# Kernel optimization log

Measured on AMD Instinct MI355X. Metric: run time of the kernel, lower is better.

Reference implementation:

```python
import jax, jax.numpy as jnp
import numpy as np

B, S, E, H = 4, 2048, 1024, 16
HD = E // H  # head_dim = 64
EPS = 1.1920928955078125e-07  # torch.finfo(float32).eps (RMSNorm eps=None default)


def _rmsnorm(x, w):
    # normalize over last dim
    ms = jnp.mean(x * x, axis=-1, keepdims=True)
    return x * jax.lax.rsqrt(ms + EPS) * w


def _rope(x, start_pos=0):
    # x: [B, H, S, HD]; interleaved (even/odd) rotary embedding
    seq_len = x.shape[-2]
    inv_freq = 1.0 / (10000.0 ** (jnp.arange(0, HD, 2, dtype=jnp.float32) / HD))  # [HD/2]
    t = jnp.arange(start_pos, start_pos + seq_len, dtype=jnp.float32)  # [S]
    freqs = t[:, None] * inv_freq[None, :]  # [S, HD/2]
    cos = jnp.cos(freqs)[None, None]  # [1,1,S,HD/2]
    sin = jnp.sin(freqs)[None, None]
    x1 = x[..., 0::2]
    x2 = x[..., 1::2]
    o1 = x1 * cos - x2 * sin
    o2 = x1 * sin + x2 * cos
    # stack(..., -1).flatten(-2) -> re-interleave
    return jnp.stack((o1, o2), axis=-1).reshape(x.shape)


def setup_inputs() -> dict:
    key = jax.random.key(0)
    k1, k2, k3, k4 = jax.random.split(key, 4)
    lim = 1.0 / np.sqrt(E)
    return {
        "q": jax.random.normal(k1, (B, S, E), jnp.float32),
        "k": jax.random.normal(k2, (B, S, E), jnp.float32),
        "v": jax.random.normal(k3, (B, S, E), jnp.float32),
        "q_norm_w": jnp.ones((HD,), jnp.float32),
        "k_norm_w": jnp.ones((HD,), jnp.float32),
        "proj_w": jax.random.uniform(k4, (E, E), jnp.float32, -lim, lim),
        "proj_b": jnp.zeros((E,), jnp.float32),
    }


def reference(q, k, v, q_norm_w, k_norm_w, proj_w, proj_b):
    b, s, _ = q.shape
    scale = HD ** -0.5
    # [B,S,E] -> [B,H,S,HD]
    qh = q.reshape(b, s, H, HD).transpose(0, 2, 1, 3)
    kh = k.reshape(b, s, H, HD).transpose(0, 2, 1, 3)
    vh = v.reshape(b, s, H, HD).transpose(0, 2, 1, 3)
    # per-head QK RMSNorm then RoPE
    qh = _rope(_rmsnorm(qh, q_norm_w))
    kh = _rope(_rmsnorm(kh, k_norm_w))
    # explicit attention (no mask path)
    scores = jnp.einsum("bhqd,bhkd->bhqk", qh, kh) * scale  # [B,H,S,S]
    attn = jax.nn.softmax(scores, axis=-1)
    ctx = jnp.einsum("bhqk,bhkd->bhqd", attn, vh)
    ctx = ctx.transpose(0, 2, 1, 3).reshape(b, s, E)
    return ctx @ proj_w.T + proj_b
```

## Files before the change

kernel.cpp:

```cpp
#include <hip/hip_runtime.h>
#include <hip/hip_bf16.h>
#include <cstdint>

#define B_ 4
#define S_ 2048
#define E_ 1024
#define H_ 16
#define HD_ 64
#define EPS_ 1.1920928955078125e-07f

typedef __attribute__((ext_vector_type(8))) short shortx8;
typedef __attribute__((ext_vector_type(4))) float floatx4;
typedef __attribute__((ext_vector_type(8))) _Float16 halfx8;
typedef __attribute__((ext_vector_type(2))) __fp16 fp16x2;

#define C1_ 0.18033688068389154f

__global__ __launch_bounds__(256) void prep(
    const float* __restrict__ q, const float* __restrict__ k,
    const float* __restrict__ v,
    const float* __restrict__ qw, const float* __restrict__ kw,
    const float* __restrict__ pw,
    __hip_bfloat16* __restrict__ qh, __hip_bfloat16* __restrict__ kh,
    _Float16* __restrict__ vt, __hip_bfloat16* __restrict__ wb)
{
    __shared__ _Float16 tile[64][72];
    const int bid = blockIdx.x;
    const int tid = threadIdx.x;

    if (bid < 16384) {
        const size_t PT = (size_t)B_ * S_ * E_ / 4;
        size_t t = (size_t)bid * 256 + tid;
        const bool is_k = (t >= PT);
        if (is_k) t -= PT;

        const int row = (int)(t >> 8);
        const int b   = row / S_;
        const int s   = row % S_;
        const int grp = (int)(t & 255);
        const int h   = grp >> 4;
        const int dl  = (grp & 15) * 4;

        const float* __restrict__ src = is_k ? k : q;
        const float* __restrict__ w   = is_k ? kw : qw;
        __hip_bfloat16* __restrict__ dst = is_k ? kh : qh;

        const float4 x  = ((const float4*)src)[t];
        const float4 wv = ((const float4*)w)[grp & 15];

        float ss = x.x * x.x + x.y * x.y + x.z * x.z + x.w * x.w;
#pragma unroll
        for (int m = 1; m < 16; m <<= 1) ss += __shfl_xor(ss, m);
        float r = rsqrtf(ss * (1.0f / HD_) + EPS_);
        if (!is_k) r *= C1_;

        const float xn0 = x.x * r * wv.x;
        const float xn1 = x.y * r * wv.y;
        const float xn2 = x.z * r * wv.z;
        const float xn3 = x.w * r * wv.w;

        const float L2I = 0.41524101186092029f;
        const int   i0  = dl >> 1;
        const float f0  = (float)s * __builtin_amdgcn_exp2f(-(float)i0 * L2I);
        const float f1  = (float)s * __builtin_amdgcn_exp2f(-(float)(i0 + 1) * L2I);
        const float c0 = __cosf(f0), sn0 = __sinf(f0);
        const float c1 = __cosf(f1), sn1 = __sinf(f1);

        __hip_bfloat16 pk[4];
        pk[0] = __float2bfloat16(xn0 * c0 - xn1 * sn0);
        pk[1] = __float2bfloat16(xn0 * sn0 + xn1 * c0);
        pk[2] = __float2bfloat16(xn2 * c1 - xn3 * sn1);
        pk[3] = __float2bfloat16(xn2 * sn1 + xn3 * c1);
        *(ushort4*)(dst + ((size_t)((b * H_ + h) * S_ + s)) * HD_ + dl) =
            *(const ushort4*)pk;
    } else if (bid < 18432) {
        const int bb2 = bid - 16384;
        const int s0  = (bb2 & 31) * 64;
        const int bh  = bb2 >> 5;
        const int b   = bh >> 4, h = bh & 15;
        {
            const int sl = tid >> 2;
            const int o  = sl;
            const int n  = (o & 32) | (((o >> 2) & 3) << 3) |
                           (((o >> 4) & 1) << 2) | (o & 3);
            const int d0 = (tid & 3) * 16;
            const float* __restrict__ src =
                v + ((size_t)(b * S_ + s0 + sl)) * E_ + h * HD_ + d0;
            float4 f0 = ((const float4*)src)[0];
            float4 f1 = ((const float4*)src)[1];
            float4 f2 = ((const float4*)src)[2];
            float4 f3 = ((const float4*)src)[3];
            float vals[16] = {f0.x,f0.y,f0.z,f0.w, f1.x,f1.y,f1.z,f1.w,
                              f2.x,f2.y,f2.z,f2.w, f3.x,f3.y,f3.z,f3.w};
#pragma unroll
            for (int j = 0; j < 16; ++j)
                tile[d0 + j][n] = (_Float16)vals[j];
        }
        __syncthreads();
        {
            const int d  = tid >> 2;
            const int sg = (tid & 3) * 16;
            _Float16* __restrict__ dst =
                vt + ((size_t)(bh * HD_ + d)) * S_ + s0 + sg;
            ((uint4*)dst)[0] = *(const uint4*)&tile[d][sg];
            ((uint4*)dst)[1] = *(const uint4*)&tile[d][sg + 8];
        }
    } else {
        const int i = (bid - 18432) * 256 + tid;
        float4 f = ((const float4*)pw)[i];
        wb[4 * i + 0] = __float2bfloat16(f.x);
        wb[4 * i + 1] = __float2bfloat16(f.y);
        wb[4 * i + 2] = __float2bfloat16(f.z);
        wb[4 * i + 3] = __float2bfloat16(f.w);
    }
}

__global__ __launch_bounds__(256, 4) void attn(
    const __hip_bfloat16* __restrict__ qh, const __hip_bfloat16* __restrict__ kh,
    const _Float16* __restrict__ vt, __hip_bfloat16* __restrict__ ctx)
{
    __shared__ __hip_bfloat16 Kt[128][72];
    __shared__ _Float16       Vt[64][152];

    const int bid  = blockIdx.x;
    const int slot = bid >> 3;
    const int bh   = ((bid & 7) << 3) | (slot & 7);
    const int q0   = (slot >> 3) * 128;
    const int tid  = threadIdx.x;
    const int wv   = tid >> 6;
    const int lane = tid & 63;
    const int l16  = lane & 15;
    const int quad = lane >> 4;
    const int b    = bh >> 4, h = bh & 15;

    shortx8 aq[2][2];
#pragma unroll
    for (int mh = 0; mh < 2; ++mh) {
        const __hip_bfloat16* qbase =
            qh + ((size_t)bh * S_ + q0 + wv * 32 + mh * 16 + l16) * HD_;
        aq[mh][0] = *(const shortx8*)(qbase + quad * 8);
        aq[mh][1] = *(const shortx8*)(qbase + 32 + quad * 8);
    }

    const halfx8 ones = {(_Float16)1.f, (_Float16)1.f, (_Float16)1.f, (_Float16)1.f,
                         (_Float16)1.f, (_Float16)1.f, (_Float16)1.f, (_Float16)1.f};

    floatx4 O[2][4] = {};
    floatx4 O5[2]   = {};

    const __hip_bfloat16* __restrict__ kbase = kh + (size_t)bh * S_ * HD_;
    const _Float16* __restrict__ vbase = vt + (size_t)bh * HD_ * S_;

    const int sr = tid >> 1, sc = (tid & 1) * 32;
    const int vr = tid >> 2, vc = (tid & 3) * 32;

    uint4 gk0, gk1, gk2, gk3, gv0, gv1, gv2, gv3;
    {
        const uint4* kp = (const uint4*)(kbase + (size_t)sr * HD_ + sc);
        gk0 = kp[0]; gk1 = kp[1]; gk2 = kp[2]; gk3 = kp[3];
        const uint4* vp = (const uint4*)(vbase + (size_t)vr * S_ + vc);
        gv0 = vp[0]; gv1 = vp[1]; gv2 = vp[2]; gv3 = vp[3];
    }

    for (int kt = 0; kt < S_ / 128; ++kt) {
        *(uint4*)&Kt[sr][sc]      = gk0;
        *(uint4*)&Kt[sr][sc + 8]  = gk1;
        *(uint4*)&Kt[sr][sc + 16] = gk2;
        *(uint4*)&Kt[sr][sc + 24] = gk3;
        *(uint4*)&Vt[vr][vc]      = gv0;
        *(uint4*)&Vt[vr][vc + 8]  = gv1;
        *(uint4*)&Vt[vr][vc + 16] = gv2;
        *(uint4*)&Vt[vr][vc + 24] = gv3;
        __syncthreads();

        if (kt + 1 < S_ / 128) {
            const uint4* kp = (const uint4*)(kbase +
                (size_t)((kt + 1) * 128 + sr) * HD_ + sc);
            gk0 = kp[0]; gk1 = kp[1]; gk2 = kp[2]; gk3 = kp[3];
        }

#pragma unroll
        for (int hk = 0; hk < 2; ++hk) {
            floatx4 s4[2][4];
            __builtin_amdgcn_s_setprio(1);
#pragma unroll
            for (int nt = 0; nt < 4; ++nt) {
                const shortx8 kb0 =
                    *(const shortx8*)&Kt[hk * 64 + nt * 16 + l16][quad * 8];
                const shortx8 kb1 =
                    *(const shortx8*)&Kt[hk * 64 + nt * 16 + l16][32 + quad * 8];
#pragma unroll
                for (int mh = 0; mh < 2; ++mh) {
                    floatx4 c = {0.f, 0.f, 0.f, 0.f};
                    c = __builtin_amdgcn_mfma_f32_16x16x32_bf16(kb0, aq[mh][0], c, 0, 0, 0);
                    c = __builtin_amdgcn_mfma_f32_16x16x32_bf16(kb1, aq[mh][1], c, 0, 0, 0);
                    s4[mh][nt] = c;
                }
            }
            __builtin_amdgcn_s_setprio(0);

            halfx8 bb[2][2];
#pragma unroll
            for (int mh = 0; mh < 2; ++mh)
#pragma unroll
                for (int f = 0; f < 2; ++f) {
                    union { fp16x2 h2[4]; halfx8 h8; } u;
                    u.h2[0] = __builtin_amdgcn_cvt_pkrtz(
                        __builtin_amdgcn_exp2f(s4[mh][2 * f][0]),
                        __builtin_amdgcn_exp2f(s4[mh][2 * f][1]));
                    u.h2[1] = __builtin_amdgcn_cvt_pkrtz(
                        __builtin_amdgcn_exp2f(s4[mh][2 * f][2]),
                        __builtin_amdgcn_exp2f(s4[mh][2 * f][3]));
                    u.h2[2] = __builtin_amdgcn_cvt_pkrtz(
                        __builtin_amdgcn_exp2f(s4[mh][2 * f + 1][0]),
                        __builtin_amdgcn_exp2f(s4[mh][2 * f + 1][1]));
                    u.h2[3] = __builtin_amdgcn_cvt_pkrtz(
                        __builtin_amdgcn_exp2f(s4[mh][2 * f + 1][2]),
                        __builtin_amdgcn_exp2f(s4[mh][2 * f + 1][3]));
                    bb[mh][f] = u.h8;
                }

            if (hk == 0 && kt + 1 < S_ / 128) {
                const uint4* vp = (const uint4*)(vbase +
                    (size_t)vr * S_ + (kt + 1) * 128 + vc);
                gv0 = vp[0]; gv1 = vp[1]; gv2 = vp[2]; gv3 = vp[3];
            }

            __builtin_amdgcn_s_setprio(1);
#pragma unroll
            for (int mh = 0; mh < 2; ++mh) {
                O5[mh] = __builtin_amdgcn_mfma_f32_16x16x32_f16(ones, bb[mh][0], O5[mh], 0, 0, 0);
                O5[mh] = __builtin_amdgcn_mfma_f32_16x16x32_f16(ones, bb[mh][1], O5[mh], 0, 0, 0);
            }

#pragma unroll
            for (int dt = 0; dt < 4; ++dt) {
                const _Float16* vrow = &Vt[dt * 16 + l16][hk * 64];
                const halfx8 A0 = *(const halfx8*)(vrow + quad * 8);
                const halfx8 A1 = *(const halfx8*)(vrow + 32 + quad * 8);
#pragma unroll
                for (int mh = 0; mh < 2; ++mh) {
                    O[mh][dt] = __builtin_amdgcn_mfma_f32_16x16x32_f16(
                        A0, bb[mh][0], O[mh][dt], 0, 0, 0);
                    O[mh][dt] = __builtin_amdgcn_mfma_f32_16x16x32_f16(
                        A1, bb[mh][1], O[mh][dt], 0, 0, 0);
                }
            }
            __builtin_amdgcn_s_setprio(0);
        }
        __syncthreads();
    }

#pragma unroll
    for (int mh = 0; mh < 2; ++mh) {
        const float inv = 1.0f / O5[mh][0];
        const int s = q0 + wv * 32 + mh * 16 + l16;
        __hip_bfloat16* cb = ctx + ((size_t)(b * S_ + s)) * E_ + h * HD_;
#pragma unroll
        for (int dt = 0; dt < 4; ++dt) {
            __hip_bfloat16 pk[4];
#pragma unroll
            for (int r = 0; r < 4; ++r)
                pk[r] = __float2bfloat16(O[mh][dt][r] * inv);
            *(ushort4*)(cb + dt * 16 + quad * 4) = *(const ushort4*)pk;
        }
    }
}

__global__ __launch_bounds__(256) void proj(
    const __hip_bfloat16* __restrict__ ctx, const __hip_bfloat16* __restrict__ wb,
    const float* __restrict__ bias, float* __restrict__ out)
{
    __shared__ __hip_bfloat16 As[128][72];
    __shared__ __hip_bfloat16 Bs[128][72];

    const int bid  = blockIdx.x;
    const int slot = bid >> 3;
    const int mblk = ((bid & 7) << 3) | (slot & 7);
    const int nblk = slot >> 3;
    const int m0 = mblk * 128;
    const int n0 = nblk * 128;
    const int tid  = threadIdx.x;
    const int wv   = tid >> 6;
    const int lane = tid & 63;
    const int l16  = lane & 15;
    const int quad = lane >> 4;
    const int wr   = (wv >> 1) * 64;
    const int wc   = (wv & 1) * 64;

    const int srow = tid >> 1;
    const int scol = (tid & 1) * 32;

    floatx4 acc[4][4] = {};

    for (int k0 = 0; k0 < E_; k0 += 64) {
        const uint4* ap = (const uint4*)(ctx + (size_t)(m0 + srow) * E_ + k0 + scol);
        const uint4* bp = (const uint4*)(wb  + (size_t)(n0 + srow) * E_ + k0 + scol);
        uint4 a0 = ap[0], a1 = ap[1], a2 = ap[2], a3 = ap[3];
        uint4 b0 = bp[0], b1 = bp[1], b2 = bp[2], b3 = bp[3];
        *(uint4*)&As[srow][scol]      = a0;
        *(uint4*)&As[srow][scol + 8]  = a1;
        *(uint4*)&As[srow][scol + 16] = a2;
        *(uint4*)&As[srow][scol + 24] = a3;
        *(uint4*)&Bs[srow][scol]      = b0;
        *(uint4*)&Bs[srow][scol + 8]  = b1;
        *(uint4*)&Bs[srow][scol + 16] = b2;
        *(uint4*)&Bs[srow][scol + 24] = b3;
        __syncthreads();

#pragma unroll
        for (int ks = 0; ks < 2; ++ks) {
            shortx8 af[4], bf[4];
#pragma unroll
            for (int mt = 0; mt < 4; ++mt)
                af[mt] = *(const shortx8*)&As[wr + mt * 16 + l16][ks * 32 + quad * 8];
#pragma unroll
            for (int nt = 0; nt < 4; ++nt)
                bf[nt] = *(const shortx8*)&Bs[wc + nt * 16 + l16][ks * 32 + quad * 8];

#pragma unroll
            for (int mt = 0; mt < 4; ++mt)
#pragma unroll
                for (int nt = 0; nt < 4; ++nt)
                    acc[mt][nt] = __builtin_amdgcn_mfma_f32_16x16x32_bf16(
                        af[mt], bf[nt], acc[mt][nt], 0, 0, 0);
        }
        __syncthreads();
    }

#pragma unroll
    for (int nt = 0; nt < 4; ++nt) {
        const float bv = bias[n0 + wc + nt * 16 + l16];
#pragma unroll
        for (int mt = 0; mt < 4; ++mt)
#pragma unroll
            for (int r = 0; r < 4; ++r) {
                const int mrow = m0 + wr + mt * 16 + quad * 4 + r;
                const int ncol = n0 + wc + nt * 16 + l16;
                out[(size_t)mrow * E_ + ncol] = acc[mt][nt][r] + bv;
            }
    }
}

extern "C" void kernel_launch(void* const* d_in, const int* in_sizes, int n_in,
                              void* d_out, int out_size, void* d_ws, size_t ws_size,
                              hipStream_t stream)
{
    const float* q  = (const float*)d_in[0];
    const float* k  = (const float*)d_in[1];
    const float* v  = (const float*)d_in[2];
    const float* qw = (const float*)d_in[3];
    const float* kw = (const float*)d_in[4];
    const float* pw = (const float*)d_in[5];
    const float* pb = (const float*)d_in[6];
    float* out = (float*)d_out;

    char* ws = (char*)d_ws;
    const size_t SEG = (size_t)B_ * H_ * S_ * HD_ * 2;
    __hip_bfloat16* qh  = (__hip_bfloat16*)(ws);
    __hip_bfloat16* kh  = (__hip_bfloat16*)(ws + SEG);
    _Float16*       vt  = (_Float16*)(ws + 2 * SEG);
    __hip_bfloat16* ctx = (__hip_bfloat16*)(ws + 3 * SEG);
    __hip_bfloat16* wbp = (__hip_bfloat16*)(ws + 4 * SEG);

    prep<<<dim3(19456), 256, 0, stream>>>(q, k, v, qw, kw, pw, qh, kh, vt, wbp);
    attn<<<dim3(1024), 256, 0, stream>>>(qh, kh, vt, ctx);
    proj<<<dim3(512), 256, 0, stream>>>(ctx, wbp, pb, out);
}
```

Measured before the change: 273.1 us.

## Drop register prefetch of K/V tiles and interleave QK MFMA with exp per half

Removes the register-staged prefetch of the next K and V tiles. Each iteration now loads its K/V tile from global memory and stores it straight to LDS before the barrier. The QK score computation is also split into two halves, so the exp/convert of one half follows its MFMAs directly. The aim is to lower register pressure and gain occupancy or interleave MFMA with transcendental work. The cost is exposed global load latency, since loads no longer overlap compute within a wave.

Result: faster. 248.1 us (-9.2%).

```diff
diff --git a/kernel.cpp b/kernel.cpp
--- a/kernel.cpp
+++ b/kernel.cpp
@@ -154,76 +154,67 @@
     const int sr = tid >> 1, sc = (tid & 1) * 32;
     const int vr = tid >> 2, vc = (tid & 3) * 32;
 
-    uint4 gk0, gk1, gk2, gk3, gv0, gv1, gv2, gv3;
-    {
-        const uint4* kp = (const uint4*)(kbase + (size_t)sr * HD_ + sc);
-        gk0 = kp[0]; gk1 = kp[1]; gk2 = kp[2]; gk3 = kp[3];
-        const uint4* vp = (const uint4*)(vbase + (size_t)vr * S_ + vc);
-        gv0 = vp[0]; gv1 = vp[1]; gv2 = vp[2]; gv3 = vp[3];
-    }
-
     for (int kt = 0; kt < S_ / 128; ++kt) {
-        *(uint4*)&Kt[sr][sc]      = gk0;
-        *(uint4*)&Kt[sr][sc + 8]  = gk1;
-        *(uint4*)&Kt[sr][sc + 16] = gk2;
-        *(uint4*)&Kt[sr][sc + 24] = gk3;
-        *(uint4*)&Vt[vr][vc]      = gv0;
-        *(uint4*)&Vt[vr][vc + 8]  = gv1;
-        *(uint4*)&Vt[vr][vc + 16] = gv2;
-        *(uint4*)&Vt[vr][vc + 24] = gv3;
-        __syncthreads();
-
-        if (kt + 1 < S_ / 128) {
+        {
             const uint4* kp = (const uint4*)(kbase +
-                (size_t)((kt + 1) * 128 + sr) * HD_ + sc);
-            gk0 = kp[0]; gk1 = kp[1]; gk2 = kp[2]; gk3 = kp[3];
-        }
+                (size_t)(kt * 128 + sr) * HD_ + sc);
+            uint4 k0 = kp[0], k1 = kp[1], k2 = kp[2], k3 = kp[3];
+            *(uint4*)&Kt[sr][sc]      = k0;
+            *(uint4*)&Kt[sr][sc + 8]  = k1;
+            *(uint4*)&Kt[sr][sc + 16] = k2;
+            *(uint4*)&Kt[sr][sc + 24] = k3;
+        }
+        {
+            const uint4* vp = (const uint4*)(vbase +
+                (size_t)vr * S_ + kt * 128 + vc);
+            uint4 v0 = vp[0], v1 = vp[1], v2 = vp[2], v3 = vp[3];
+            *(uint4*)&Vt[vr][vc]      = v0;
+            *(uint4*)&Vt[vr][vc + 8]  = v1;
+            *(uint4*)&Vt[vr][vc + 16] = v2;
+            *(uint4*)&Vt[vr][vc + 24] = v3;
+        }
+        __syncthreads();
 
 #pragma unroll
         for (int hk = 0; hk < 2; ++hk) {
-            floatx4 s4[2][4];
-            __builtin_amdgcn_s_setprio(1);
-#pragma unroll
-            for (int nt = 0; nt < 4; ++nt) {
-                const shortx8 kb0 =
-                    *(const shortx8*)&Kt[hk * 64 + nt * 16 + l16][quad * 8];
-                const shortx8 kb1 =
-                    *(const shortx8*)&Kt[hk * 64 + nt * 16 + l16][32 + quad * 8];
+            halfx8 bb[2][2];
+#pragma unroll
+            for (int f = 0; f < 2; ++f) {
+                floatx4 s4p[2][2];
+                __builtin_amdgcn_s_setprio(1);
+#pragma unroll
+                for (int nt2 = 0; nt2 < 2; ++nt2) {
+                    const int nt = 2 * f + nt2;
+                    const shortx8 kb0 =
+                        *(const shortx8*)&Kt[hk * 64 + nt * 16 + l16][quad * 8];
+                    const shortx8 kb1 =
+                        *(const shortx8*)&Kt[hk * 64 + nt * 16 + l16][32 + quad * 8];
+#pragma unroll
+                    for (int mh = 0; mh < 2; ++mh) {
+                        floatx4 c = {0.f, 0.f, 0.f, 0.f};
+                        c = __builtin_amdgcn_mfma_f32_16x16x32_bf16(kb0, aq[mh][0], c, 0, 0, 0);
+                        c = __builtin_amdgcn_mfma_f32_16x16x32_bf16(kb1, aq[mh][1], c, 0, 0, 0);
+                        s4p[mh][nt2] = c;
+                    }
+                }
+                __builtin_amdgcn_s_setprio(0);
 #pragma unroll
                 for (int mh = 0; mh < 2; ++mh) {
-                    floatx4 c = {0.f, 0.f, 0.f, 0.f};
-                    c = __builtin_amdgcn_mfma_f32_16x16x32_bf16(kb0, aq[mh][0], c, 0, 0, 0);
-                    c = __builtin_amdgcn_mfma_f32_16x16x32_bf16(kb1, aq[mh][1], c, 0, 0, 0);
-                    s4[mh][nt] = c;
-                }
-            }
-            __builtin_amdgcn_s_setprio(0);
-
-            halfx8 bb[2][2];
-#pragma unroll
-            for (int mh = 0; mh < 2; ++mh)
-#pragma unroll
-                for (int f = 0; f < 2; ++f) {
                     union { fp16x2 h2[4]; halfx8 h8; } u;
                     u.h2[0] = __builtin_amdgcn_cvt_pkrtz(
-                        __builtin_amdgcn_exp2f(s4[mh][2 * f][0]),
-                        __builtin_amdgcn_exp2f(s4[mh][2 * f][1]));
+                        __builtin_amdgcn_exp2f(s4p[mh][0][0]),
+                        __builtin_amdgcn_exp2f(s4p[mh][0][1]));
                     u.h2[1] = __builtin_amdgcn_cvt_pkrtz(
-                        __builtin_amdgcn_exp2f(s4[mh][2 * f][2]),
-                        __builtin_amdgcn_exp2f(s4[mh][2 * f][3]));
+                        __builtin_amdgcn_exp2f(s4p[mh][0][2]),
+                        __builtin_amdgcn_exp2f(s4p[mh][0][3]));
                     u.h2[2] = __builtin_amdgcn_cvt_pkrtz(
-                        __builtin_amdgcn_exp2f(s4[mh][2 * f + 1][0]),
-                        __builtin_amdgcn_exp2f(s4[mh][2 * f + 1][1]));
+                        __builtin_amdgcn_exp2f(s4p[mh][1][0]),
+                        __builtin_amdgcn_exp2f(s4p[mh][1][1]));
                     u.h2[3] = __builtin_amdgcn_cvt_pkrtz(
-                        __builtin_amdgcn_exp2f(s4[mh][2 * f + 1][2]),
-                        __builtin_amdgcn_exp2f(s4[mh][2 * f + 1][3]));
+                        __builtin_amdgcn_exp2f(s4p[mh][1][2]),
+                        __builtin_amdgcn_exp2f(s4p[mh][1][3]));
                     bb[mh][f] = u.h8;
                 }
-
-            if (hk == 0 && kt + 1 < S_ / 128) {
-                const uint4* vp = (const uint4*)(vbase +
-                    (size_t)vr * S_ + (kt + 1) * 128 + vc);
-                gv0 = vp[0]; gv1 = vp[1]; gv2 = vp[2]; gv3 = vp[3];
             }
 
             __builtin_amdgcn_s_setprio(1);
```
